# Kernel optimization log

Hardware: AMD Instinct MI355X
Metric: run time of the kernel (lower is better)

## Reference

```python
import jax, jax.numpy as jnp
import numpy as np
from jax import lax

IN_CH, OUT_CH, K, B, T = 64, 128, 3, 64, 2048
BN_EPS = 1e-5


def setup_inputs() -> dict:
    key = jax.random.key(0)
    ks = jax.random.split(key, 10)
    s_dw = 1.0 / np.sqrt(K)            # torch Conv1d init scale (fan_in = in_ch/groups * k = k)
    s_pw = 1.0 / np.sqrt(IN_CH)        # fan_in = in_ch * 1
    s_l = 1.0 / np.sqrt(OUT_CH)        # torch LSTM init scale
    return {
        "x": jax.random.normal(ks[0], (B, IN_CH, T), dtype=jnp.float32),
        "dw_w": jax.random.uniform(ks[1], (IN_CH, 1, K), jnp.float32, -s_dw, s_dw),
        "dw_b": jax.random.uniform(ks[2], (IN_CH,), jnp.float32, -s_dw, s_dw),
        "bn_gamma": jnp.ones((IN_CH,), jnp.float32),
        "bn_beta": jnp.zeros((IN_CH,), jnp.float32),
        "bn_mean": jnp.zeros((IN_CH,), jnp.float32),
        "bn_var": jnp.ones((IN_CH,), jnp.float32),
        "pw_w": jax.random.uniform(ks[3], (OUT_CH, IN_CH), jnp.float32, -s_pw, s_pw),
        "pw_b": jax.random.uniform(ks[4], (OUT_CH,), jnp.float32, -s_pw, s_pw),
        "w_ih": jax.random.uniform(ks[5], (4 * OUT_CH, OUT_CH), jnp.float32, -s_l, s_l),
        "w_hh": jax.random.uniform(ks[6], (4 * OUT_CH, OUT_CH), jnp.float32, -s_l, s_l),
        "b_ih": jax.random.uniform(ks[7], (4 * OUT_CH,), jnp.float32, -s_l, s_l),
        "b_hh": jax.random.uniform(ks[8], (4 * OUT_CH,), jnp.float32, -s_l, s_l),
    }


def _block(x, dw_w, dw_b, bn_gamma, bn_beta, bn_mean, bn_var,
           pw_w, pw_b, w_ih, w_hh, b_ih, b_hh):
    in_ch = x.shape[1]
    # depthwise conv1d, padding=1 (same)
    h = lax.conv_general_dilated(
        x, dw_w, window_strides=(1,), padding=[(1, 1)],
        dimension_numbers=("NCH", "OIH", "NCH"), feature_group_count=in_ch)
    h = h + dw_b[None, :, None]
    # BatchNorm1d (inference: running stats) + ReLU + residual
    inv = bn_gamma / jnp.sqrt(bn_var + BN_EPS)
    h = (h - bn_mean[None, :, None]) * inv[None, :, None] + bn_beta[None, :, None]
    h = jax.nn.relu(h) + x
    # pointwise 1x1 conv: [B, in_ch, T] -> [B, out_ch, T]
    h = jnp.einsum("bct,oc->bot", h, pw_w) + pw_b[None, :, None]
    # LSTM over time (batch_first); dropouti inactive at inference
    xs = h.transpose(2, 0, 1)                       # [T, B, H]
    gx = jnp.einsum("tbh,gh->tbg", xs, w_ih) + (b_ih + b_hh)  # precompute input gates
    H = w_hh.shape[1]
    h0 = jnp.zeros((xs.shape[1], H), xs.dtype)
    c0 = jnp.zeros_like(h0)

    def step(carry, gx_t):
        h_prev, c_prev = carry
        gates = gx_t + h_prev @ w_hh.T              # [B, 4H]
        i, f, g, o = jnp.split(gates, 4, axis=-1)   # torch gate order i,f,g,o
        i = jax.nn.sigmoid(i)
        f = jax.nn.sigmoid(f)
        g = jnp.tanh(g)
        o = jax.nn.sigmoid(o)
        c = f * c_prev + i * g
        h_t = o * jnp.tanh(c)
        return (h_t, c), h_t

    _, hs = lax.scan(step, (h0, c0), gx)            # hs: [T, B, H]
    return hs.transpose(1, 2, 0)                    # [B, H, T]


def reference(x, dw_w, dw_b, bn_gamma, bn_beta, bn_mean, bn_var,
              pw_w, pw_b, w_ih, w_hh, b_ih, b_hh):
    return _block(x, dw_w, dw_b, bn_gamma, bn_beta, bn_mean, bn_var,
                  pw_w, pw_b, w_ih, w_hh, b_ih, b_hh)
```

## Files before the change

kernel.cpp:

```cpp
#include <hip/hip_runtime.h>
#include <hip/hip_bf16.h>
#include <hip/hip_fp16.h>

typedef _Float16 f16x8 __attribute__((ext_vector_type(8)));
typedef float    f32x4 __attribute__((ext_vector_type(4)));

#define T_LEN 2048
#define T_CHUNK 1024

__device__ inline f32x4 vfma4(f32x4 a, f32x4 b, f32x4 c) {
#if __has_builtin(__builtin_elementwise_fma)
  return __builtin_elementwise_fma(a, b, c);
#else
  return a * b + c;
#endif
}

__global__ __launch_bounds__(256) void k1_front(
    const float* __restrict__ x, const float* __restrict__ dw_w, const float* __restrict__ dw_b,
    const float* __restrict__ bn_g, const float* __restrict__ bn_b, const float* __restrict__ bn_m,
    const float* __restrict__ bn_v, const float* __restrict__ pw_w, const float* __restrict__ pw_b,
    float* __restrict__ hpw, int tc0) {
  __shared__ float xs[64][130];
  __shared__ float ys[64][128];
  __shared__ float wT[64][128];
  __shared__ float4 sc[64];
  const int b = blockIdx.y;
  const int t0l = blockIdx.x * 128;
  const int t0 = tc0 + t0l;
  const int tid = threadIdx.x;

  for (int idx = tid; idx < 64 * 130; idx += 256) {
    int c = idx / 130, tt = idx % 130;
    int gt = t0 + tt - 1;
    xs[c][tt] = (gt >= 0 && gt < T_LEN) ? x[((size_t)b * 64 + c) * T_LEN + gt] : 0.f;
  }
  for (int idx = tid; idx < 64 * 128; idx += 256) {
    int o = idx & 127, c = idx >> 7;
    wT[c][o] = pw_w[o * 64 + c];
  }
  if (tid < 64) {
    int c = tid;
    float inv = bn_g[c] * rsqrtf(bn_v[c] + 1e-5f);
    sc[c] = make_float4(dw_w[c * 3 + 0] * inv, dw_w[c * 3 + 1] * inv, dw_w[c * 3 + 2] * inv,
                        (dw_b[c] - bn_m[c]) * inv + bn_b[c]);
  }
  __syncthreads();
  for (int idx = tid; idx < 64 * 128; idx += 256) {
    int c = idx >> 7, j = idx & 127;
    float4 s = sc[c];
    float v = s.x * xs[c][j] + s.y * xs[c][j + 1] + s.z * xs[c][j + 2] + s.w;
    ys[c][j] = fmaxf(v, 0.f) + xs[c][j + 1];
  }
  __syncthreads();
  const int o = tid & 127, tg = tid >> 7, tb = tg * 64;
  float acc[64];
#pragma unroll
  for (int i = 0; i < 64; ++i) acc[i] = 0.f;
  for (int c = 0; c < 64; ++c) {
    float w = wT[c][o];
#pragma unroll
    for (int i = 0; i < 64; ++i) acc[i] = fmaf(w, ys[c][tb + i], acc[i]);
  }
  float pb = pw_b[o];
#pragma unroll
  for (int i = 0; i < 64; ++i) {
    hpw[((size_t)(t0l + tb + i) * 64 + b) * 128 + o] = acc[i] + pb;
  }
}

__global__ __launch_bounds__(256) void k2_gx(
    const float* __restrict__ hpw, const float* __restrict__ w_ih,
    const float* __restrict__ b_ih, const float* __restrict__ b_hh, float* __restrict__ gx) {
  __shared__ __align__(16) _Float16 As_hi[128 * 128];
  __shared__ __align__(16) _Float16 As_lo[128 * 128];
  __shared__ __align__(16) _Float16 Bs_hi[128 * 128];
  __shared__ __align__(16) _Float16 Bs_lo[128 * 128];
  const int m0 = blockIdx.x * 128;
  const int n0 = blockIdx.y * 128;
  const int tid = threadIdx.x;

#pragma unroll
  for (int it = 0; it < 8; ++it) {
    int idx = it * 256 + tid;
    int r = idx >> 4, u = idx & 15;
    const float* src = hpw + ((size_t)(m0 + r) << 7) + u * 8;
    f16x8 hi, lo;
#pragma unroll
    for (int j = 0; j < 8; ++j) {
      float v = src[j];
      _Float16 h = (_Float16)v;
      hi[j] = h;
      lo[j] = (_Float16)((v - (float)h) * 2048.0f);
    }
    int du = (u ^ (r & 7)) * 16;
    *(f16x8*)((char*)As_hi + r * 256 + du) = hi;
    *(f16x8*)((char*)As_lo + r * 256 + du) = lo;
  }
#pragma unroll
  for (int it = 0; it < 8; ++it) {
    int idx = it * 256 + tid;
    int r = idx >> 4, u = idx & 15;
    const float* src = w_ih + (size_t)(n0 + r) * 128 + u * 8;
    f16x8 hi, lo;
#pragma unroll
    for (int j = 0; j < 8; ++j) {
      float v = src[j];
      _Float16 h = (_Float16)v;
      hi[j] = h;
      lo[j] = (_Float16)((v - (float)h) * 2048.0f);
    }
    int du = (u ^ (r & 7)) * 16;
    *(f16x8*)((char*)Bs_hi + r * 256 + du) = hi;
    *(f16x8*)((char*)Bs_lo + r * 256 + du) = lo;
  }
  __syncthreads();

  const int lane = tid & 63, wv = tid >> 6;
  const int wm = (wv >> 1) * 64, wn = (wv & 1) * 64;
  f32x4 acc[4][4] = {};
  f32x4 accc[4][4] = {};
#pragma unroll
  for (int kk = 0; kk < 4; ++kk) {
    f16x8 ah[4], al[4], bh[4], bl[4];
#pragma unroll
    for (int mi = 0; mi < 4; ++mi) {
      int row = wm + mi * 16 + (lane & 15);
      int u = kk * 4 + (lane >> 4);
      int off = row * 256 + ((u ^ (row & 7)) * 16);
      ah[mi] = *(const f16x8*)((const char*)As_hi + off);
      al[mi] = *(const f16x8*)((const char*)As_lo + off);
    }
#pragma unroll
    for (int ni = 0; ni < 4; ++ni) {
      int row = wn + ni * 16 + (lane & 15);
      int u = kk * 4 + (lane >> 4);
      int off = row * 256 + ((u ^ (row & 7)) * 16);
      bh[ni] = *(const f16x8*)((const char*)Bs_hi + off);
      bl[ni] = *(const f16x8*)((const char*)Bs_lo + off);
    }
#pragma unroll
    for (int mi = 0; mi < 4; ++mi)
#pragma unroll
      for (int ni = 0; ni < 4; ++ni) {
        acc[mi][ni]  = __builtin_amdgcn_mfma_f32_16x16x32_f16(ah[mi], bh[ni], acc[mi][ni], 0, 0, 0);
        accc[mi][ni] = __builtin_amdgcn_mfma_f32_16x16x32_f16(ah[mi], bl[ni], accc[mi][ni], 0, 0, 0);
        accc[mi][ni] = __builtin_amdgcn_mfma_f32_16x16x32_f16(al[mi], bh[ni], accc[mi][ni], 0, 0, 0);
      }
  }
  const float ks = 1.0f / 2048.0f;
#pragma unroll
  for (int ni = 0; ni < 4; ++ni) {
    int col = n0 + wn + ni * 16 + (lane & 15);
    float bias = b_ih[col] + b_hh[col];
#pragma unroll
    for (int mi = 0; mi < 4; ++mi) {
#pragma unroll
      for (int j = 0; j < 4; ++j) {
        int row = m0 + wm + mi * 16 + (lane >> 4) * 4 + j;
        gx[(size_t)row * 512 + col] = acc[mi][ni][j] + accc[mi][ni][j] * ks + bias;
      }
    }
  }
}

__global__ __launch_bounds__(512) void k3_lstm(
    const float* __restrict__ gx, const float* __restrict__ w_hh, float* __restrict__ out,
    int tc0, int nt, float* __restrict__ carry_h, float* __restrict__ carry_c, int first) {
  const int b = blockIdx.x;
  const int g = threadIdx.x;
  __shared__ __align__(16) float h_lds[128];
  __shared__ float gates[512];

  f32x4 wv[32];
  const float* wr = w_hh + (size_t)g * 128;
#pragma unroll
  for (int k = 0; k < 32; ++k) wv[k] = *(const f32x4*)(wr + 4 * k);

  float cst = 0.f;
  if (g < 128) {
    h_lds[g] = first ? 0.f : carry_h[b * 128 + g];
    if (!first) cst = carry_c[b * 128 + g];
  }
  float gxn = gx[(size_t)b * 512 + g];
  __syncthreads();

  for (int t = 0; t < nt; ++t) {
    int tn = (t + 1 < nt) ? (t + 1) : t;
    float gx_next = gx[((size_t)tn * 64 + b) * 512 + g];

    f32x4 a = {0.f, 0.f, 0.f, 0.f};
    const f32x4* h4 = (const f32x4*)h_lds;
#pragma unroll
    for (int k = 0; k < 32; ++k) {
      a = vfma4(wv[k], h4[k], a);
    }
    float pre = gxn + ((a[0] + a[1]) + (a[2] + a[3]));
    float act = ((g >> 7) == 2) ? tanhf(pre) : 1.f / (1.f + expf(-pre));
    gates[g] = act;
    gxn = gx_next;
    __syncthreads();

    if (g < 128) {
      float i_ = gates[g], f_ = gates[g + 128], gg = gates[g + 256], o_ = gates[g + 384];
      cst = fmaf(f_, cst, i_ * gg);
      float h = o_ * tanhf(cst);
      h_lds[g] = h;
      out[((size_t)b * 128 + g) * T_LEN + tc0 + t] = h;
    }
    __syncthreads();
  }
  if (g < 128) {
    carry_h[b * 128 + g] = h_lds[g];
    carry_c[b * 128 + g] = cst;
  }
}

extern "C" void kernel_launch(void* const* d_in, const int* in_sizes, int n_in,
                              void* d_out, int out_size, void* d_ws, size_t ws_size,
                              hipStream_t stream) {
  const float* x    = (const float*)d_in[0];
  const float* dw_w = (const float*)d_in[1];
  const float* dw_b = (const float*)d_in[2];
  const float* bn_g = (const float*)d_in[3];
  const float* bn_b = (const float*)d_in[4];
  const float* bn_m = (const float*)d_in[5];
  const float* bn_v = (const float*)d_in[6];
  const float* pw_w = (const float*)d_in[7];
  const float* pw_b = (const float*)d_in[8];
  const float* w_ih = (const float*)d_in[9];
  const float* w_hh = (const float*)d_in[10];
  const float* b_ih = (const float*)d_in[11];
  const float* b_hh = (const float*)d_in[12];
  float* out = (float*)d_out;

  float* hpw = (float*)d_ws;
  float* gx  = (float*)((char*)d_ws + (size_t)33554432);
  float* ch  = (float*)((char*)d_ws + (size_t)167772160);
  float* cc  = (float*)((char*)d_ws + (size_t)167804928);

  for (int c = 0; c < 2; ++c) {
    int tc0 = c * T_CHUNK;
    k1_front<<<dim3(8, 64), 256, 0, stream>>>(x, dw_w, dw_b, bn_g, bn_b, bn_m, bn_v, pw_w, pw_b, hpw, tc0);
    k2_gx<<<dim3(512, 4), 256, 0, stream>>>(hpw, w_ih, b_ih, b_hh, gx);
    k3_lstm<<<64, 512, 0, stream>>>(gx, w_hh, out, tc0, T_CHUNK, ch, cc, c == 0);
  }
}
```

Before: 2.046 ms.

## Halve LSTM block threads, use fast activations, widen gx tiles, adapt chunking

```diff
diff --git a/kernel.cpp b/kernel.cpp
--- a/kernel.cpp
+++ b/kernel.cpp
@@ -6,7 +6,6 @@
 typedef float    f32x4 __attribute__((ext_vector_type(4)));
 
 #define T_LEN 2048
-#define T_CHUNK 1024
 
 __device__ inline f32x4 vfma4(f32x4 a, f32x4 b, f32x4 c) {
 #if __has_builtin(__builtin_elementwise_fma)
@@ -14,6 +13,14 @@
 #else
   return a * b + c;
 #endif
+}
+
+__device__ inline float fast_sigmoid(float x) {
+  return __builtin_amdgcn_rcpf(1.f + __expf(-x));
+}
+__device__ inline float fast_tanh(float x) {
+  float e = __expf(2.f * x);
+  return 1.f - 2.f * __builtin_amdgcn_rcpf(e + 1.f);
 }
 
 __global__ __launch_bounds__(256) void k1_front(
@@ -77,7 +84,7 @@
   __shared__ __align__(16) _Float16 Bs_hi[128 * 128];
   __shared__ __align__(16) _Float16 Bs_lo[128 * 128];
   const int m0 = blockIdx.x * 128;
-  const int n0 = blockIdx.y * 128;
+  const int nbase = blockIdx.y * 256;
   const int tid = threadIdx.x;
 
 #pragma unroll
@@ -97,122 +104,147 @@
     *(f16x8*)((char*)As_hi + r * 256 + du) = hi;
     *(f16x8*)((char*)As_lo + r * 256 + du) = lo;
   }
-#pragma unroll
-  for (int it = 0; it < 8; ++it) {
-    int idx = it * 256 + tid;
-    int r = idx >> 4, u = idx & 15;
-    const float* src = w_ih + (size_t)(n0 + r) * 128 + u * 8;
-    f16x8 hi, lo;
-#pragma unroll
-    for (int j = 0; j < 8; ++j) {
-      float v = src[j];
-      _Float16 h = (_Float16)v;
-      hi[j] = h;
-      lo[j] = (_Float16)((v - (float)h) * 2048.0f);
-    }
-    int du = (u ^ (r & 7)) * 16;
-    *(f16x8*)((char*)Bs_hi + r * 256 + du) = hi;
-    *(f16x8*)((char*)Bs_lo + r * 256 + du) = lo;
-  }
-  __syncthreads();
 
   const int lane = tid & 63, wv = tid >> 6;
   const int wm = (wv >> 1) * 64, wn = (wv & 1) * 64;
-  f32x4 acc[4][4] = {};
-  f32x4 accc[4][4] = {};
-#pragma unroll
-  for (int kk = 0; kk < 4; ++kk) {
-    f16x8 ah[4], al[4], bh[4], bl[4];
-#pragma unroll
-    for (int mi = 0; mi < 4; ++mi) {
-      int row = wm + mi * 16 + (lane & 15);
-      int u = kk * 4 + (lane >> 4);
-      int off = row * 256 + ((u ^ (row & 7)) * 16);
-      ah[mi] = *(const f16x8*)((const char*)As_hi + off);
-      al[mi] = *(const f16x8*)((const char*)As_lo + off);
-    }
+
+  for (int ns = 0; ns < 2; ++ns) {
+    const int n0 = nbase + ns * 128;
+#pragma unroll
+    for (int it = 0; it < 8; ++it) {
+      int idx = it * 256 + tid;
+      int r = idx >> 4, u = idx & 15;
+      const float* src = w_ih + (size_t)(n0 + r) * 128 + u * 8;
+      f16x8 hi, lo;
+#pragma unroll
+      for (int j = 0; j < 8; ++j) {
+        float v = src[j];
+        _Float16 h = (_Float16)v;
+        hi[j] = h;
+        lo[j] = (_Float16)((v - (float)h) * 2048.0f);
+      }
+      int du = (u ^ (r & 7)) * 16;
+      *(f16x8*)((char*)Bs_hi + r * 256 + du) = hi;
+      *(f16x8*)((char*)Bs_lo + r * 256 + du) = lo;
+    }
+    __syncthreads();
+
+    f32x4 acc[4][4] = {};
+    f32x4 accc[4][4] = {};
+#pragma unroll
+    for (int kk = 0; kk < 4; ++kk) {
+      f16x8 ah[4], al[4], bh[4], bl[4];
+#pragma unroll
+      for (int mi = 0; mi < 4; ++mi) {
+        int row = wm + mi * 16 + (lane & 15);
+        int u = kk * 4 + (lane >> 4);
+        int off = row * 256 + ((u ^ (row & 7)) * 16);
+        ah[mi] = *(const f16x8*)((const char*)As_hi + off);
+        al[mi] = *(const f16x8*)((const char*)As_lo + off);
+      }
+#pragma unroll
+      for (int ni = 0; ni < 4; ++ni) {
+        int row = wn + ni * 16 + (lane & 15);
+        int u = kk * 4 + (lane >> 4);
+        int off = row * 256 + ((u ^ (row & 7)) * 16);
+        bh[ni] = *(const f16x8*)((const char*)Bs_hi + off);
+        bl[ni] = *(const f16x8*)((const char*)Bs_lo + off);
+      }
+#pragma unroll
+      for (int mi = 0; mi < 4; ++mi)
+#pragma unroll
+        for (int ni = 0; ni < 4; ++ni) {
+          acc[mi][ni]  = __builtin_amdgcn_mfma_f32_16x16x32_f16(ah[mi], bh[ni], acc[mi][ni], 0, 0, 0);
+          accc[mi][ni] = __builtin_amdgcn_mfma_f32_16x16x32_f16(ah[mi], bl[ni], accc[mi][ni], 0, 0, 0);
+          accc[mi][ni] = __builtin_amdgcn_mfma_f32_16x16x32_f16(al[mi], bh[ni], accc[mi][ni], 0, 0, 0);
+        }
+    }
+    const float ks = 1.0f / 2048.0f;
 #pragma unroll
     for (int ni = 0; ni < 4; ++ni) {
-      int row = wn + ni * 16 + (lane & 15);
-      int u = kk * 4 + (lane >> 4);
-      int off = row * 256 + ((u ^ (row & 7)) * 16);
-      bh[ni] = *(const f16x8*)((const char*)Bs_hi + off);
-      bl[ni] = *(const f16x8*)((const char*)Bs_lo + off);
-    }
-#pragma unroll
-    for (int mi = 0; mi < 4; ++mi)
-#pragma unroll
-      for (int ni = 0; ni < 4; ++ni) {
-        acc[mi][ni]  = __builtin_amdgcn_mfma_f32_16x16x32_f16(ah[mi], bh[ni], acc[mi][ni], 0, 0, 0);
-        accc[mi][ni] = __builtin_amdgcn_mfma_f32_16x16x32_f16(ah[mi], bl[ni], accc[mi][ni], 0, 0, 0);
-        accc[mi][ni] = __builtin_amdgcn_mfma_f32_16x16x32_f16(al[mi], bh[ni], accc[mi][ni], 0, 0, 0);
-      }
-  }
-  const float ks = 1.0f / 2048.0f;
-#pragma unroll
-  for (int ni = 0; ni < 4; ++ni) {
-    int col = n0 + wn + ni * 16 + (lane & 15);
-    float bias = b_ih[col] + b_hh[col];
-#pragma unroll
-    for (int mi = 0; mi < 4; ++mi) {
-#pragma unroll
-      for (int j = 0; j < 4; ++j) {
-        int row = m0 + wm + mi * 16 + (lane >> 4) * 4 + j;
-        gx[(size_t)row * 512 + col] = acc[mi][ni][j] + accc[mi][ni][j] * ks + bias;
-      }
-    }
-  }
-}
-
-__global__ __launch_bounds__(512) void k3_lstm(
+      int col = n0 + wn + ni * 16 + (lane & 15);
+      float bias = b_ih[col] + b_hh[col];
+#pragma unroll
+      for (int mi = 0; mi < 4; ++mi) {
+#pragma unroll
+        for (int j = 0; j < 4; ++j) {
+          int row = m0 + wm + mi * 16 + (lane >> 4) * 4 + j;
+          gx[(size_t)row * 512 + col] = acc[mi][ni][j] + accc[mi][ni][j] * ks + bias;
+        }
+      }
+    }
+    __syncthreads();
+  }
+}
+
+__global__ __launch_bounds__(256, 1) void k3_lstm(
     const float* __restrict__ gx, const float* __restrict__ w_hh, float* __restrict__ out,
     int tc0, int nt, float* __restrict__ carry_h, float* __restrict__ carry_c, int first) {
   const int b = blockIdx.x;
-  const int g = threadIdx.x;
+  const int t0 = threadIdx.x;
+  const int rA = t0;
+  const int rB = t0 + 256;
   __shared__ __align__(16) float h_lds[128];
   __shared__ float gates[512];
 
-  f32x4 wv[32];
-  const float* wr = w_hh + (size_t)g * 128;
-#pragma unroll
-  for (int k = 0; k < 32; ++k) wv[k] = *(const f32x4*)(wr + 4 * k);
+  f32x4 wA[32], wB[32];
+  {
+    const float* wa = w_hh + (size_t)rA * 128;
+    const float* wb = w_hh + (size_t)rB * 128;
+#pragma unroll
+    for (int k = 0; k < 32; ++k) {
+      wA[k] = *(const f32x4*)(wa + 4 * k);
+      wB[k] = *(const f32x4*)(wb + 4 * k);
+    }
+  }
 
   float cst = 0.f;
-  if (g < 128) {
-    h_lds[g] = first ? 0.f : carry_h[b * 128 + g];
-    if (!first) cst = carry_c[b * 128 + g];
-  }
-  float gxn = gx[(size_t)b * 512 + g];
+  if (t0 < 128) {
+    h_lds[t0] = first ? 0.f : carry_h[b * 128 + t0];
+    if (!first) cst = carry_c[b * 128 + t0];
+  }
+  float gxA = gx[(size_t)b * 512 + rA];
+  float gxB = gx[(size_t)b * 512 + rB];
   __syncthreads();
 
   for (int t = 0; t < nt; ++t) {
     int tn = (t + 1 < nt) ? (t + 1) : t;
-    float gx_next = gx[((size_t)tn * 64 + b) * 512 + g];
-
-    f32x4 a = {0.f, 0.f, 0.f, 0.f};
+    float gxA_n = gx[((size_t)tn * 64 + b) * 512 + rA];
+    float gxB_n = gx[((size_t)tn * 64 + b) * 512 + rB];
+
+    f32x4 a0 = {0,0,0,0}, a1 = {0,0,0,0}, b0 = {0,0,0,0}, b1 = {0,0,0,0};
     const f32x4* h4 = (const f32x4*)h_lds;
 #pragma unroll
-    for (int k = 0; k < 32; ++k) {
-      a = vfma4(wv[k], h4[k], a);
-    }
-    float pre = gxn + ((a[0] + a[1]) + (a[2] + a[3]));
-    float act = ((g >> 7) == 2) ? tanhf(pre) : 1.f / (1.f + expf(-pre));
-    gates[g] = act;
-    gxn = gx_next;
-    __syncthreads();
-
-    if (g < 128) {
-      float i_ = gates[g], f_ = gates[g + 128], gg = gates[g + 256], o_ = gates[g + 384];
+    for (int k = 0; k < 16; ++k) {
+      f32x4 h0 = h4[2 * k], h1v = h4[2 * k + 1];
+      a0 = vfma4(wA[2 * k], h0, a0);
+      a1 = vfma4(wA[2 * k + 1], h1v, a1);
+      b0 = vfma4(wB[2 * k], h0, b0);
+      b1 = vfma4(wB[2 * k + 1], h1v, b1);
+    }
+    f32x4 sa = a0 + a1, sb = b0 + b1;
+    float preA = gxA + ((sa[0] + sa[1]) + (sa[2] + sa[3]));
+    float preB = gxB + ((sb[0] + sb[1]) + (sb[2] + sb[3]));
+    float actA = fast_sigmoid(preA);
+    float actB = (t0 < 128) ? fast_tanh(preB) : fast_sigmoid(preB);
+    gates[rA] = actA;
+    gates[rB] = actB;
+    gxA = gxA_n;
+    gxB = gxB_n;
+    __syncthreads();
+
+    if (t0 < 128) {
+      float i_ = gates[t0], f_ = gates[t0 + 128], gg = gates[t0 + 256], o_ = gates[t0 + 384];
       cst = fmaf(f_, cst, i_ * gg);
-      float h = o_ * tanhf(cst);
-      h_lds[g] = h;
-      out[((size_t)b * 128 + g) * T_LEN + tc0 + t] = h;
-    }
-    __syncthreads();
-  }
-  if (g < 128) {
-    carry_h[b * 128 + g] = h_lds[g];
-    carry_c[b * 128 + g] = cst;
+      float h = o_ * fast_tanh(cst);
+      h_lds[t0] = h;
+      out[((size_t)b * 128 + t0) * T_LEN + tc0 + t] = h;
+    }
+    __syncthreads();
+  }
+  if (t0 < 128) {
+    carry_h[b * 128 + t0] = h_lds[t0];
+    carry_c[b * 128 + t0] = cst;
   }
 }
 
@@ -234,15 +266,22 @@
   const float* b_hh = (const float*)d_in[12];
   float* out = (float*)d_out;
 
+  const size_t need_full = (size_t)T_LEN * 64 * 128 * 4 + (size_t)T_LEN * 64 * 512 * 4 + 65536;
+  const int nchunks = (ws_size >= need_full) ? 1 : 2;
+  const int nt = T_LEN / nchunks;
+
+  const size_t hpw_bytes = (size_t)nt * 64 * 128 * 4;
+  const size_t gx_bytes  = (size_t)nt * 64 * 512 * 4;
   float* hpw = (float*)d_ws;
-  float* gx  = (float*)((char*)d_ws + (size_t)33554432);
-  float* ch  = (float*)((char*)d_ws + (size_t)167772160);
-  float* cc  = (float*)((char*)d_ws + (size_t)167804928);
-
-  for (int c = 0; c < 2; ++c) {
-    int tc0 = c * T_CHUNK;
-    k1_front<<<dim3(8, 64), 256, 0, stream>>>(x, dw_w, dw_b, bn_g, bn_b, bn_m, bn_v, pw_w, pw_b, hpw, tc0);
-    k2_gx<<<dim3(512, 4), 256, 0, stream>>>(hpw, w_ih, b_ih, b_hh, gx);
-    k3_lstm<<<64, 512, 0, stream>>>(gx, w_hh, out, tc0, T_CHUNK, ch, cc, c == 0);
-  }
-}
+  float* gx  = (float*)((char*)d_ws + hpw_bytes);
+  float* ch  = (float*)((char*)d_ws + hpw_bytes + gx_bytes);
+  float* cc  = ch + 8192;
+
+  for (int c = 0; c < nchunks; ++c) {
+    int tc0 = c * nt;
+    k1_front<<<dim3(nt / 128, 64), 256, 0, stream>>>(x, dw_w, dw_b, bn_g, bn_b, bn_m, bn_v,
+                                                     pw_w, pw_b, hpw, tc0);
+    k2_gx<<<dim3(nt / 2, 2), 256, 0, stream>>>(hpw, w_ih, b_ih, b_hh, gx);
+    k3_lstm<<<64, 256, 0, stream>>>(gx, w_hh, out, tc0, nt, ch, cc, c == 0);
+  }
+}
```

Result: slower. 2.906 ms (+42.0%).
